# Optimization experiments

Measured on AMD Instinct MI355X. Metric: run time of the kernel, lower is better.

The kernel has to match this reference:

```python
import jax, jax.numpy as jnp
import numpy as np

MARGIN = 0.36
ALPHA_INIT = 0.0
ALPHA_MOMENT = 0.995
LAMBDA_CLEAN = 1.0
LAMBDA_ADV = 1.0
EPS_SIM = 0.01
BIG = 99999.0

CNT = 8192
DIM = 128


def dot_to_dist(dot, alpha, eps=1e-12):
    return alpha * (1.0 - dot) + (1.0 - alpha) * jnp.sqrt(2.0 * (1.0 - dot) + eps)


def find_hard_negatives(dmat):
    # HyNet-style mining: dmat[i, j] = 'distance' between a_i and p_j.
    # Positive pair is the diagonal; hardest negative for triplet i is the min
    # over row i (a_i vs other p) or column i (p_i vs other a), diag excluded.
    cnt = dmat.shape[0]
    dm = dmat + jnp.eye(cnt, dtype=dmat.dtype) * BIG  # mask diagonal
    row_min = dm.min(axis=1)
    row_arg = jnp.argmin(dm, axis=1)
    col_min = dm.min(axis=0)
    col_arg = jnp.argmin(dm, axis=0)
    idx_a = jnp.arange(cnt)
    idx_p = idx_a + cnt
    # indices into cat([a, p]): hardest p lives at j+cnt, hardest a at j
    idx_n = jnp.where(row_min < col_min, row_arg + cnt, col_arg)
    return idx_a, idx_p, idx_n


def estimate_alpha(dots, labels, weights):
    # Vectorized over the 200-point alpha grid (original: Python loop).
    alphas = jnp.arange(-1.0, 1.0, 0.01, dtype=dots.dtype)  # [K=200]
    one_minus = (1.0 - dots)[None, :]                        # [1, N]
    sq = jnp.sqrt(2.0 * (1.0 - dots) + 1e-12)[None, :]       # [1, N]
    dists = alphas[:, None] * one_minus + (1.0 - alphas)[:, None] * sq  # [K, N]
    n = dists.shape[1]
    mean = dists.mean(axis=1, keepdims=True)
    std = jnp.sqrt(((dists - mean) ** 2).sum(axis=1, keepdims=True) / (n - 1))  # unbiased, as torch.std
    probs = jax.nn.sigmoid(-(dists - mean) / std)
    bce = jnp.mean(-labels * jnp.log(probs) * weights
                   - (1.0 - labels) * jnp.log(1.0 - probs) * weights, axis=1)  # [K]
    return alphas[jnp.argmin(bce)]


def _rowdot(x, y):
    return jnp.sum(x * y, axis=1)


def setup_inputs() -> dict:
    key = jax.random.key(0)
    k1, k2, k3 = jax.random.split(key, 3)
    descs = jax.random.normal(k1, (6 * CNT, DIM), dtype=jnp.float32)
    l_a_adv = jax.random.uniform(k2, (CNT,), dtype=jnp.float32)
    l_p_adv = jax.random.uniform(k3, (CNT,), dtype=jnp.float32)
    return {"descs": descs, "l_a_adv": l_a_adv, "l_p_adv": l_p_adv}


def reference(descs, l_a_adv, l_p_adv):
    cnt = descs.shape[0] // 6
    xn = descs / jnp.linalg.norm(descs, axis=1, keepdims=True)
    a     = xn[0 * cnt:1 * cnt]
    p     = xn[1 * cnt:2 * cnt]
    a_rec = xn[2 * cnt:3 * cnt]
    p_rec = xn[3 * cnt:4 * cnt]
    a_adv = xn[4 * cnt:5 * cnt]
    p_adv = xn[5 * cnt:6 * cnt]

    # hard-negative mining (no_grad in original)
    sg = jax.lax.stop_gradient
    smat_ap   = sg(a)     @ sg(p).T       # [cnt, cnt]
    smat_arpa = sg(a_rec) @ sg(p_adv).T
    smat_aapr = sg(a_adv) @ sg(p_rec).T
    idx_a, idx_p, idx_n                = find_hard_negatives(1.0 / smat_ap + EPS_SIM)
    idx_a_arpa, idx_p_arpa, idx_n_arpa = find_hard_negatives(1.0 / smat_arpa + EPS_SIM)
    idx_a_aapr, idx_p_aapr, idx_n_aapr = find_hard_negatives(1.0 / smat_aapr + EPS_SIM)

    xn_ap   = jnp.concatenate([a, p], axis=0)
    xn_arpa = jnp.concatenate([a_rec, p_adv], axis=0)
    xn_aapr = jnp.concatenate([a_adv, p_rec], axis=0)

    pos_ap   = _rowdot(xn_ap[idx_a],        xn_ap[idx_p])
    neg_ap   = _rowdot(xn_ap[idx_a],        xn_ap[idx_n])
    pos_arpa = _rowdot(xn_arpa[idx_a_arpa], xn_arpa[idx_p_arpa])
    neg_arpa = _rowdot(xn_arpa[idx_a_arpa], xn_arpa[idx_n_arpa])
    pos_aapr = _rowdot(xn_aapr[idx_a_aapr], xn_aapr[idx_p_aapr])
    neg_aapr = _rowdot(xn_aapr[idx_a_aapr], xn_aapr[idx_n_aapr])

    acos = lambda d: jnp.arccos(jnp.clip(d, -1.0, 1.0))
    mask = (MARGIN + acos(pos_ap) - acos(neg_ap) > 0).astype(descs.dtype)

    # alpha estimation (no_grad)
    dots = sg(jnp.concatenate([pos_ap, pos_arpa, pos_aapr, neg_ap, neg_arpa, neg_aapr]))
    labels = jnp.concatenate([jnp.ones(cnt * 3, descs.dtype), jnp.zeros(cnt * 3, descs.dtype)])
    weights = jnp.concatenate([
        jnp.full((cnt,), LAMBDA_CLEAN, descs.dtype), jnp.full((2 * cnt,), LAMBDA_ADV, descs.dtype),
        jnp.full((cnt,), LAMBDA_CLEAN, descs.dtype), jnp.full((2 * cnt,), LAMBDA_ADV, descs.dtype)])
    alpha_opt = estimate_alpha(dots, labels, weights)
    alpha = ALPHA_INIT * ALPHA_MOMENT + alpha_opt * (1.0 - ALPHA_MOMENT)

    loss_triplet_clean = jnp.mean((dot_to_dist(pos_ap, alpha) - dot_to_dist(neg_ap, alpha)) * mask) * LAMBDA_CLEAN
    loss_triplet_arpa = jnp.mean((l_p_adv * dot_to_dist(pos_arpa, alpha) - dot_to_dist(neg_arpa, alpha)) * mask) * LAMBDA_ADV
    loss_triplet_aapr = jnp.mean((l_a_adv * dot_to_dist(pos_aapr, alpha) - dot_to_dist(neg_aapr, alpha)) * mask) * LAMBDA_ADV
    loss = jnp.mean(jnp.stack([loss_triplet_clean, loss_triplet_arpa, loss_triplet_aapr]))

    l_mean = (l_a_adv.mean() + l_p_adv.mean()) / 2.0
    mask_ratio = mask.sum() / cnt
    return (loss, loss_triplet_clean, loss_triplet_arpa, loss_triplet_aapr, l_mean, alpha, alpha_opt, mask_ratio)
```

## Files before the change

kernel.cpp:

```cpp
#include <hip/hip_runtime.h>
#include <stdint.h>

#define CNT 8192
#define DIM 128

typedef unsigned long long u64;
typedef unsigned int u32;

#define OFF_POS     ((size_t)0)
#define OFF_NEG     (OFF_POS + (size_t)3*CNT*4)
#define OFF_ROWPART (OFF_NEG + (size_t)3*CNT*4)
#define OFF_COLPART (OFF_ROWPART + (size_t)3*64*CNT*4)
#define OFF_U       (OFF_COLPART + (size_t)3*64*CNT*4)
#define OFF_V       (OFF_U + (size_t)6*CNT*4)
#define OFF_MPART   (OFF_V + (size_t)6*CNT*4)
#define OFF_AMEAN   (OFF_MPART + (size_t)6144*5*4)
#define OFF_AISTD   (OFF_AMEAN + (size_t)1024)
#define OFF_PSUM    (OFF_AISTD + (size_t)1024)
#define OFF_XNB     (OFF_PSUM + (size_t)8192)

typedef __attribute__((ext_vector_type(8))) short short8;
typedef __attribute__((ext_vector_type(4))) float f32x4;

__device__ __forceinline__ float fract1(float x){
#if __has_builtin(__builtin_amdgcn_fractf)
  return __builtin_amdgcn_fractf(x);
#else
  return x - floorf(x);
#endif
}
__device__ __forceinline__ u32 umax2(u32 a, u32 b){ return a > b ? a : b; }
__device__ __forceinline__ u32 umax3(u32 a, u32 b, u32 c){ u32 t = a > b ? a : b; return t > c ? t : c; }

__device__ __forceinline__ float block_sum(float x, float* red, int tid){
  #pragma unroll
  for (int m=1;m<64;m<<=1) x += __shfl_xor(x, m, 64);
  if ((tid & 63) == 0) red[tid>>6] = x;
  __syncthreads();
  const float r = red[0]+red[1]+red[2]+red[3];
  __syncthreads();
  return r;
}

__global__ __launch_bounds__(256) void knorm(const float* __restrict__ in,
                                             unsigned int* __restrict__ xnb32){
  const int row  = blockIdx.x*4 + (threadIdx.x>>6);
  const int lane = threadIdx.x & 63;
  const float2 v = *(const float2*)(in + (size_t)row*DIM + lane*2);
  float ss = v.x*v.x + v.y*v.y;
  #pragma unroll
  for (int m=1;m<64;m<<=1) ss += __shfl_xor(ss, m, 64);
  const float sc = ((row & CNT) ? 1.0f : 0.25f) / sqrtf(ss);
  unsigned int ux = __float_as_uint(v.x*sc), uy = __float_as_uint(v.y*sc);
  ux = (ux + 0x7FFFu + ((ux>>16)&1u)) >> 16;
  uy = (uy + 0x7FFFu + ((uy>>16)&1u)) >> 16;
  xnb32[(size_t)row*64 + lane] = ux | (uy<<16);
}

__global__ __launch_bounds__(256) void kgemm(const unsigned short* __restrict__ xnb,
    u32* __restrict__ rowpart, u32* __restrict__ colpart){
  __shared__ __align__(16) unsigned short S[4][128*32];
  const int pair = blockIdx.z;
  const int xo3[3] = {0, 2*CNT, 4*CNT};
  const int yo3[3] = {CNT, 5*CNT, 3*CNT};
  const unsigned short* __restrict__ X = xnb + (size_t)xo3[pair]*DIM;
  const unsigned short* __restrict__ Y = xnb + (size_t)yo3[pair]*DIM;
  const int brow = blockIdx.y*128, bcol = blockIdx.x*128;
  const int tid = threadIdx.x, lane = tid & 63, wid = tid >> 6;
  const int wr = wid >> 1, wc = wid & 1;
  const int lrow = lane & 15, kgrp = lane >> 4;

  const int j0 = wid*2, j1 = wid*2 + 1;
  const int r0 = j0*16 + (lane>>2), r1 = j1*16 + (lane>>2);
  const int slog = (lane&3) ^ ((lane>>3)&3);
  const unsigned short* gx0 = X + (size_t)(brow + r0)*DIM + slog*8;
  const unsigned short* gx1 = X + (size_t)(brow + r1)*DIM + slog*8;
  const unsigned short* gy0 = Y + (size_t)(bcol + r0)*DIM + slog*8;
  const unsigned short* gy1 = Y + (size_t)(bcol + r1)*DIM + slog*8;

#define STAGEC(c) do{ \
    unsigned short* LX = S[((c)&1)*2]; \
    unsigned short* LY = S[((c)&1)*2 + 1]; \
    __builtin_amdgcn_global_load_lds((const __attribute__((address_space(1))) void*)(gx0 + (c)*32), \
        (__attribute__((address_space(3))) void*)(LX + j0*512), 16, 0, 0); \
    __builtin_amdgcn_global_load_lds((const __attribute__((address_space(1))) void*)(gx1 + (c)*32), \
        (__attribute__((address_space(3))) void*)(LX + j1*512), 16, 0, 0); \
    __builtin_amdgcn_global_load_lds((const __attribute__((address_space(1))) void*)(gy0 + (c)*32), \
        (__attribute__((address_space(3))) void*)(LY + j0*512), 16, 0, 0); \
    __builtin_amdgcn_global_load_lds((const __attribute__((address_space(1))) void*)(gy1 + (c)*32), \
        (__attribute__((address_space(3))) void*)(LY + j1*512), 16, 0, 0); \
  }while(0)

  f32x4 acc[4][4];
  #pragma unroll
  for (int m=0;m<4;m++)
    #pragma unroll
    for (int n=0;n<4;n++)
      acc[m][n] = (f32x4){0.f,0.f,0.f,0.f};

  STAGEC(0);
  __syncthreads();

  const int swzb = ((lrow>>1)&3) << 4;
  #pragma unroll
  for (int c=0;c<4;c++){
    if (c<3) STAGEC(c+1);
    const char* LX = (const char*)S[(c&1)*2];
    const char* LY = (const char*)S[(c&1)*2 + 1];
    const int kb = (kgrp*16) ^ swzb;
    short8 av[4], bv[4];
    #pragma unroll
    for (int m=0;m<4;m++){
      av[m] = *(const short8*)(LX + (wr*64 + m*16 + lrow)*64 + kb);
      bv[m] = *(const short8*)(LY + (wc*64 + m*16 + lrow)*64 + kb);
    }
    #pragma unroll
    for (int m=0;m<4;m++)
      #pragma unroll
      for (int n=0;n<4;n++)
        acc[m][n] = __builtin_amdgcn_mfma_f32_16x16x32_bf16(av[m], bv[n], acc[m][n], 0, 0, 0);
    if (c<3) __syncthreads();
  }

  if (blockIdx.x == blockIdx.y && wr == wc && kgrp == (lrow >> 2)){
    #pragma unroll
    for (int r=0;r<4;r++)
      if ((lrow & 3) == r){
        #pragma unroll
        for (int m=0;m<4;m++) acc[m][m][r] = 0.0f;
      }
  }

  const int colb_loc = wc*64 + lrow;
  u32 orvr[4];
  #pragma unroll
  for (int n=0;n<4;n++) orvr[n] = (u32)(127 - colb_loc - n*16);

  u32 pkc[4] = {0u,0u,0u,0u};
  u32 rpk[16];
  #pragma unroll
  for (int m=0;m<4;m++){
    #pragma unroll
    for (int r=0;r<4;r++){
      const u32 orvc = (u32)(63 - (m*16 + kgrp*4 + r));
      u32 kb2[4];
      #pragma unroll
      for (int n=0;n<4;n++)
        kb2[n] = __float_as_uint(fract1(acc[m][n][r]));
      const u32 b0 = (kb2[0] & 0xFFFFFF80u) | orvr[0];
      const u32 b1 = (kb2[1] & 0xFFFFFF80u) | orvr[1];
      const u32 b2 = (kb2[2] & 0xFFFFFF80u) | orvr[2];
      const u32 b3 = (kb2[3] & 0xFFFFFF80u) | orvr[3];
      rpk[m*4+r] = umax2(umax3(b0, b1, b2), b3);
      const u32 c0 = (kb2[0] & 0xFFFFFFC0u) | orvc;
      const u32 c1 = (kb2[1] & 0xFFFFFFC0u) | orvc;
      const u32 c2 = (kb2[2] & 0xFFFFFFC0u) | orvc;
      const u32 c3 = (kb2[3] & 0xFFFFFFC0u) | orvc;
      pkc[0] = umax2(pkc[0], c0);
      pkc[1] = umax2(pkc[1], c1);
      pkc[2] = umax2(pkc[2], c2);
      pkc[3] = umax2(pkc[3], c3);
    }
  }

  #pragma unroll
  for (int n=0;n<4;n++){
    u32 o = (u32)__shfl_xor((int)pkc[n], 16, 64); pkc[n] = umax2(pkc[n], o);
    o = (u32)__shfl_xor((int)pkc[n], 32, 64);     pkc[n] = umax2(pkc[n], o);
  }

  __syncthreads();
  u32* rowbuf = (u32*)S;
  u32* colred = (u32*)((char*)S + 20480);
  {
    const int slot = wc*16 + lrow;
    #pragma unroll
    for (int m=0;m<4;m++)
      #pragma unroll
      for (int r=0;r<4;r++){
        const int row = wr*64 + m*16 + kgrp*4 + r;
        rowbuf[row*36 + slot] = rpk[m*4+r];
      }
    if (kgrp == 0){
      #pragma unroll
      for (int n=0;n<4;n++)
        colred[wr*128 + wc*64 + n*16 + lrow] = pkc[n];
    }
  }
  __syncthreads();

  if (tid < 128){
    const u32* base = rowbuf + tid*36;
    u32 best = 0u;
    #pragma unroll
    for (int q=0;q<8;q++){
      const uint4 t = *(const uint4*)(base + q*4);
      best = umax2(best, umax2(umax3(t.x, t.y, t.z), t.w));
    }
    const int colg = 127 - (int)(best & 127u);
    rowpart[((size_t)pair*64 + blockIdx.x)*CNT + (brow + tid)] =
        ((~best) & 0xFFFFE000u) | (u32)(bcol + colg);
  } else {
    const int c = tid - 128;
    const u32 a0 = colred[c], a1 = colred[128 + c];
    const u32 w = a1 > a0 ? a1 : a0;
    const int rloc = (a1 > a0 ? 64 : 0) + (63 - (int)(w & 63u));
    colpart[((size_t)pair*64 + blockIdx.y)*CNT + (bcol + c)] =
        ((~w) & 0xFFFFE000u) | (u32)(brow + rloc);
  }
#undef STAGEC
}

__global__ __launch_bounds__(256) void kpick(const float* __restrict__ descs,
    const u32* __restrict__ rowpart, const u32* __restrict__ colpart,
    float* __restrict__ pos, float* __restrict__ neg,
    float* __restrict__ u, float* __restrict__ v, float* __restrict__ mpart){
  __shared__ float sred[4][5];
  const int tid = threadIdx.x;
  const int w4 = tid >> 6, lane = tid & 63;
  const int e = blockIdx.x*4 + w4;
  const int p = e >> 13, i = e & (CNT-1);
  const int xo[3] = {0, 2*CNT, 4*CNT};
  const int yo[3] = {CNT, 5*CNT, 3*CNT};
  u32 rv = rowpart[((size_t)p*64 + lane)*CNT + i];
  u32 cv = colpart[((size_t)p*64 + lane)*CNT + i];
  #pragma unroll
  for (int m=1;m<64;m<<=1){
    u32 o = (u32)__shfl_xor((int)rv, m, 64); rv = o < rv ? o : rv;
    o = (u32)__shfl_xor((int)cv, m, 64);     cv = o < cv ? o : cv;
  }
  int orow;
  if ((rv & 0xFFFFE000u) < (cv & 0xFFFFE000u)) orow = yo[p] + (int)(rv & 0x1FFFu);
  else                                          orow = xo[p] + (int)(cv & 0x1FFFu);
  const float2 va = *(const float2*)(descs + (size_t)(xo[p]+i)*DIM + lane*2);
  const float2 vp = *(const float2*)(descs + (size_t)(yo[p]+i)*DIM + lane*2);
  const float2 vn = *(const float2*)(descs + (size_t)orow*DIM + lane*2);
  float saa = va.x*va.x + va.y*va.y;
  float spp = vp.x*vp.x + vp.y*vp.y;
  float snn = vn.x*vn.x + vn.y*vn.y;
  float sap = va.x*vp.x + va.y*vp.y;
  float san = va.x*vn.x + va.y*vn.y;
  #pragma unroll
  for (int m=1;m<64;m<<=1){
    saa += __shfl_xor(saa, m, 64);
    spp += __shfl_xor(spp, m, 64);
    snn += __shfl_xor(snn, m, 64);
    sap += __shfl_xor(sap, m, 64);
    san += __shfl_xor(san, m, 64);
  }
  if (lane == 0){
    const float dp = sap / (sqrtf(saa)*sqrtf(spp));
    const float dn = san / (sqrtf(saa)*sqrtf(snn));
    pos[p*CNT + i] = dp; neg[p*CNT + i] = dn;
    const float omp_ = 1.f - dp, sqp = sqrtf(2.f*omp_ + 1e-12f), up = omp_ - sqp;
    const float omn_ = 1.f - dn, sqn = sqrtf(2.f*omn_ + 1e-12f), un = omn_ - sqn;
    u[p*CNT + i] = up;           v[p*CNT + i] = sqp;
    u[3*CNT + p*CNT + i] = un;   v[3*CNT + p*CNT + i] = sqn;
    const float cup = up + 0.35f, cvp = sqp - 0.80f;
    const float cun = un + 0.35f, cvn = sqn - 0.80f;
    sred[w4][0] = up + un;
    sred[w4][1] = sqp + sqn;
    sred[w4][2] = cup*cup + cun*cun;
    sred[w4][3] = cup*cvp + cun*cvn;
    sred[w4][4] = cvp*cvp + cvn*cvn;
  }
  __syncthreads();
  if (tid < 5)
    mpart[blockIdx.x*5 + tid] = sred[0][tid] + sred[1][tid] + sred[2][tid] + sred[3][tid];
}

__global__ __launch_bounds__(256) void kmom(const float* __restrict__ mpart,
    float* __restrict__ amean, float* __restrict__ aistd){
  __shared__ float red[4];
  __shared__ float sm[5];
  const int tid = threadIdx.x;
  float a0=0.f,a1=0.f,a2=0.f,a3=0.f,a4=0.f;
  for (int i = tid; i < 6144; i += 256){
    const float* mp = mpart + (size_t)i*5;
    a0+=mp[0]; a1+=mp[1]; a2+=mp[2]; a3+=mp[3]; a4+=mp[4];
  }
  a0 = block_sum(a0, red, tid);
  a1 = block_sum(a1, red, tid);
  a2 = block_sum(a2, red, tid);
  a3 = block_sum(a3, red, tid);
  a4 = block_sum(a4, red, tid);
  if (tid == 0){ sm[0]=a0; sm[1]=a1; sm[2]=a2; sm[3]=a3; sm[4]=a4; }
  __syncthreads();
  const float N = 49152.0f;
  const float mu_u = sm[0]/N, mu_v = sm[1]/N;
  const float du = mu_u + 0.35f, dv = mu_v - 0.80f;
  const float Suu = sm[2] - N*du*du;
  const float Suv = sm[3] - N*du*dv;
  const float Svv = sm[4] - N*dv*dv;
  if (tid < 200){
    const float a = -1.0f + 0.01f*(float)tid;
    amean[tid] = a*mu_u + mu_v;
    const float var = (a*a*Suu + 2.0f*a*Suv + Svv) / 49151.0f;
    aistd[tid] = 1.0f/sqrtf(var);
  }
}

__global__ __launch_bounds__(256) void kbce(const float* __restrict__ u, const float* __restrict__ v,
    const float* __restrict__ amean, const float* __restrict__ aistd, float* __restrict__ psum){
  __shared__ float red[4];
  const int tid = threadIdx.x;
  const int a = blockIdx.x >> 3, c = blockIdx.x & 7;
  const float av = -1.0f + 0.01f*(float)a;
  const float mean = amean[a], istd = aistd[a];
  const int base = c*6144;
  float s = 0.0f;
  #pragma unroll 4
  for (int k = 0; k < 24; ++k){
    const int idx = base + k*256 + tid;
    const float z = (fmaf(av, u[idx], v[idx]) - mean) * istd;
    const float zz = (idx < 3*CNT) ? z : -z;
    s += fmaxf(zz, 0.0f) + __logf(1.0f + __expf(-fabsf(zz)));
  }
  s = block_sum(s, red, tid);
  if (tid == 0) psum[blockIdx.x] = s;
}

__global__ __launch_bounds__(256) void kfinal(const float* __restrict__ pos, const float* __restrict__ neg,
    const float* __restrict__ psum, const float* __restrict__ l_a_adv, const float* __restrict__ l_p_adv,
    float* __restrict__ out){
  __shared__ float sbce[200];
  __shared__ float sal[2];
  __shared__ float red[4];
  const int tid = threadIdx.x;
  if (tid < 200){
    float s = 0.f;
    #pragma unroll
    for (int c=0;c<8;c++) s += psum[tid*8 + c];
    sbce[tid] = s;
  }
  __syncthreads();
  if (tid == 0){
    float best = sbce[0]; int bk = 0;
    for (int k=1;k<200;k++){
      const float vv = sbce[k];
      if (vv < best){ best = vv; bk = k; }
    }
    const float aopt = -1.0f + 0.01f*(float)bk;
    sal[0] = aopt;
    sal[1] = aopt * 0.005f;
  }
  __syncthreads();
  const float alpha = sal[1];

  float sc=0.f, sar=0.f, saa=0.f, sm=0.f, sla=0.f, slp=0.f;
  for (int i = tid; i < CNT; i += 256){
    const float pap = pos[i],        nap = neg[i];
    const float par = pos[CNT+i],    nar = neg[CNT+i];
    const float paa = pos[2*CNT+i],  naa = neg[2*CNT+i];
    const float cp = fminf(fmaxf(pap, -1.0f), 1.0f);
    const float cn = fminf(fmaxf(nap, -1.0f), 1.0f);
    const float m = (0.36f + acosf(cp) - acosf(cn) > 0.0f) ? 1.0f : 0.0f;
    #define DDIST(d) (alpha*(1.0f-(d)) + (1.0f-alpha)*sqrtf(2.0f*(1.0f-(d)) + 1e-12f))
    sc  += (DDIST(pap) - DDIST(nap)) * m;
    sar += (l_p_adv[i]*DDIST(par) - DDIST(nar)) * m;
    saa += (l_a_adv[i]*DDIST(paa) - DDIST(naa)) * m;
    sm  += m;
    sla += l_a_adv[i];
    slp += l_p_adv[i];
  }
  float vals[6] = {sc, sar, saa, sm, sla, slp};
  float tot[6];
  for (int vv=0; vv<6; vv++){
    tot[vv] = block_sum(vals[vv], red, tid);
  }
  if (tid == 0){
    const float lc  = tot[0] / (float)CNT;
    const float lar = tot[1] / (float)CNT;
    const float laa = tot[2] / (float)CNT;
    out[0] = (lc + lar + laa) / 3.0f;
    out[1] = lc;
    out[2] = lar;
    out[3] = laa;
    out[4] = (tot[4]/(float)CNT + tot[5]/(float)CNT) * 0.5f;
    out[5] = sal[1];
    out[6] = sal[0];
    out[7] = tot[3] / (float)CNT;
  }
}

extern "C" void kernel_launch(void* const* d_in, const int* in_sizes, int n_in,
                              void* d_out, int out_size, void* d_ws, size_t ws_size,
                              hipStream_t stream) {
  const float* descs = (const float*)d_in[0];
  const float* l_a   = (const float*)d_in[1];
  const float* l_p   = (const float*)d_in[2];
  float* out = (float*)d_out;
  char* ws = (char*)d_ws;

  float* pos = (float*)(ws + OFF_POS);
  float* neg = (float*)(ws + OFF_NEG);
  u32* rowpart = (u32*)(ws + OFF_ROWPART);
  u32* colpart = (u32*)(ws + OFF_COLPART);
  float* u     = (float*)(ws + OFF_U);
  float* v     = (float*)(ws + OFF_V);
  float* mpart = (float*)(ws + OFF_MPART);
  float* amean = (float*)(ws + OFF_AMEAN);
  float* aistd = (float*)(ws + OFF_AISTD);
  float* psum  = (float*)(ws + OFF_PSUM);
  unsigned int* xnb32 = (unsigned int*)(ws + OFF_XNB);
  const unsigned short* xnb = (const unsigned short*)(ws + OFF_XNB);

  knorm  <<<(6*CNT)/4, 256, 0, stream>>>(descs, xnb32);
  kgemm  <<<dim3(64,64,3), 256, 0, stream>>>(xnb, rowpart, colpart);
  kpick  <<<(3*CNT)/4, 256, 0, stream>>>(descs, rowpart, colpart, pos, neg, u, v, mpart);
  kmom   <<<1, 256, 0, stream>>>(mpart, amean, aistd);
  kbce   <<<1600, 256, 0, stream>>>(u, v, amean, aistd, psum);
  kfinal <<<1, 256, 0, stream>>>(pos, neg, psum, l_a, l_p, out);
}
```

Measured before the change: 156.6 us.

## Enlarge GEMM tile to 256x128 and reuse precomputed inverse norms in pick

The similarity GEMM tile grows from 128x128 to 256x128, so each wave computes 8x4 MFMA tiles. This halves the grid rows and the column-partial buffer, and B fragments are reused across more A rows. Row results are written straight to LDS instead of being held in registers. knorm now stores each row's inverse norm, so kpick computes only two dot products per triplet instead of five reductions. The cost is more accumulator registers and LDS per block, which can lower occupancy.

```diff
diff --git a/kernel.cpp b/kernel.cpp
--- a/kernel.cpp
+++ b/kernel.cpp
@@ -11,7 +11,8 @@
 #define OFF_NEG     (OFF_POS + (size_t)3*CNT*4)
 #define OFF_ROWPART (OFF_NEG + (size_t)3*CNT*4)
 #define OFF_COLPART (OFF_ROWPART + (size_t)3*64*CNT*4)
-#define OFF_U       (OFF_COLPART + (size_t)3*64*CNT*4)
+#define OFF_RNORM   (OFF_COLPART + (size_t)3*32*CNT*4)
+#define OFF_U       (OFF_RNORM + (size_t)6*CNT*4)
 #define OFF_V       (OFF_U + (size_t)6*CNT*4)
 #define OFF_MPART   (OFF_V + (size_t)6*CNT*4)
 #define OFF_AMEAN   (OFF_MPART + (size_t)6144*5*4)
@@ -43,57 +44,65 @@
 }
 
 __global__ __launch_bounds__(256) void knorm(const float* __restrict__ in,
-                                             unsigned int* __restrict__ xnb32){
+                                             unsigned int* __restrict__ xnb32,
+                                             float* __restrict__ rnorm){
   const int row  = blockIdx.x*4 + (threadIdx.x>>6);
   const int lane = threadIdx.x & 63;
   const float2 v = *(const float2*)(in + (size_t)row*DIM + lane*2);
   float ss = v.x*v.x + v.y*v.y;
   #pragma unroll
   for (int m=1;m<64;m<<=1) ss += __shfl_xor(ss, m, 64);
-  const float sc = ((row & CNT) ? 1.0f : 0.25f) / sqrtf(ss);
+  const float rn = 1.0f / sqrtf(ss);
+  const float sc = ((row & CNT) ? 1.0f : 0.25f) * rn;
   unsigned int ux = __float_as_uint(v.x*sc), uy = __float_as_uint(v.y*sc);
   ux = (ux + 0x7FFFu + ((ux>>16)&1u)) >> 16;
   uy = (uy + 0x7FFFu + ((uy>>16)&1u)) >> 16;
   xnb32[(size_t)row*64 + lane] = ux | (uy<<16);
+  if (lane == 0) rnorm[row] = rn;
 }
 
 __global__ __launch_bounds__(256) void kgemm(const unsigned short* __restrict__ xnb,
     u32* __restrict__ rowpart, u32* __restrict__ colpart){
-  __shared__ __align__(16) unsigned short S[4][128*32];
+  __shared__ __align__(16) char LB[49152];
   const int pair = blockIdx.z;
   const int xo3[3] = {0, 2*CNT, 4*CNT};
   const int yo3[3] = {CNT, 5*CNT, 3*CNT};
   const unsigned short* __restrict__ X = xnb + (size_t)xo3[pair]*DIM;
   const unsigned short* __restrict__ Y = xnb + (size_t)yo3[pair]*DIM;
-  const int brow = blockIdx.y*128, bcol = blockIdx.x*128;
+  const int brow = blockIdx.y*256, bcol = blockIdx.x*128;
   const int tid = threadIdx.x, lane = tid & 63, wid = tid >> 6;
   const int wr = wid >> 1, wc = wid & 1;
   const int lrow = lane & 15, kgrp = lane >> 4;
 
-  const int j0 = wid*2, j1 = wid*2 + 1;
-  const int r0 = j0*16 + (lane>>2), r1 = j1*16 + (lane>>2);
+  const int rr16 = lane >> 2;
   const int slog = (lane&3) ^ ((lane>>3)&3);
-  const unsigned short* gx0 = X + (size_t)(brow + r0)*DIM + slog*8;
-  const unsigned short* gx1 = X + (size_t)(brow + r1)*DIM + slog*8;
-  const unsigned short* gy0 = Y + (size_t)(bcol + r0)*DIM + slog*8;
-  const unsigned short* gy1 = Y + (size_t)(bcol + r1)*DIM + slog*8;
+  const unsigned short* gA[4];
+  #pragma unroll
+  for (int t=0;t<4;t++) gA[t] = X + (size_t)(brow + (wid*4+t)*16 + rr16)*DIM + slog*8;
+  const unsigned short* gB[2];
+  #pragma unroll
+  for (int t=0;t<2;t++) gB[t] = Y + (size_t)(bcol + (wid*2+t)*16 + rr16)*DIM + slog*8;
 
 #define STAGEC(c) do{ \
-    unsigned short* LX = S[((c)&1)*2]; \
-    unsigned short* LY = S[((c)&1)*2 + 1]; \
-    __builtin_amdgcn_global_load_lds((const __attribute__((address_space(1))) void*)(gx0 + (c)*32), \
-        (__attribute__((address_space(3))) void*)(LX + j0*512), 16, 0, 0); \
-    __builtin_amdgcn_global_load_lds((const __attribute__((address_space(1))) void*)(gx1 + (c)*32), \
-        (__attribute__((address_space(3))) void*)(LX + j1*512), 16, 0, 0); \
-    __builtin_amdgcn_global_load_lds((const __attribute__((address_space(1))) void*)(gy0 + (c)*32), \
-        (__attribute__((address_space(3))) void*)(LY + j0*512), 16, 0, 0); \
-    __builtin_amdgcn_global_load_lds((const __attribute__((address_space(1))) void*)(gy1 + (c)*32), \
-        (__attribute__((address_space(3))) void*)(LY + j1*512), 16, 0, 0); \
+    char* LA_ = LB + ((c)&1)*16384; \
+    char* LB_ = LB + 32768 + ((c)&1)*8192; \
+    __builtin_amdgcn_global_load_lds((const __attribute__((address_space(1))) void*)(gA[0] + (c)*32), \
+        (__attribute__((address_space(3))) void*)(LA_ + (wid*4+0)*1024), 16, 0, 0); \
+    __builtin_amdgcn_global_load_lds((const __attribute__((address_space(1))) void*)(gA[1] + (c)*32), \
+        (__attribute__((address_space(3))) void*)(LA_ + (wid*4+1)*1024), 16, 0, 0); \
+    __builtin_amdgcn_global_load_lds((const __attribute__((address_space(1))) void*)(gA[2] + (c)*32), \
+        (__attribute__((address_space(3))) void*)(LA_ + (wid*4+2)*1024), 16, 0, 0); \
+    __builtin_amdgcn_global_load_lds((const __attribute__((address_space(1))) void*)(gA[3] + (c)*32), \
+        (__attribute__((address_space(3))) void*)(LA_ + (wid*4+3)*1024), 16, 0, 0); \
+    __builtin_amdgcn_global_load_lds((const __attribute__((address_space(1))) void*)(gB[0] + (c)*32), \
+        (__attribute__((address_space(3))) void*)(LB_ + (wid*2+0)*1024), 16, 0, 0); \
+    __builtin_amdgcn_global_load_lds((const __attribute__((address_space(1))) void*)(gB[1] + (c)*32), \
+        (__attribute__((address_space(3))) void*)(LB_ + (wid*2+1)*1024), 16, 0, 0); \
   }while(0)
 
-  f32x4 acc[4][4];
-  #pragma unroll
-  for (int m=0;m<4;m++)
+  f32x4 acc[8][4];
+  #pragma unroll
+  for (int m=0;m<8;m++)
     #pragma unroll
     for (int n=0;n<4;n++)
       acc[m][n] = (f32x4){0.f,0.f,0.f,0.f};
@@ -101,48 +110,56 @@
   STAGEC(0);
   __syncthreads();
 
-  const int swzb = ((lrow>>1)&3) << 4;
+  const int kb = (kgrp*16) ^ (((lrow>>1)&3) << 4);
   #pragma unroll
   for (int c=0;c<4;c++){
     if (c<3) STAGEC(c+1);
-    const char* LX = (const char*)S[(c&1)*2];
-    const char* LY = (const char*)S[(c&1)*2 + 1];
-    const int kb = (kgrp*16) ^ swzb;
-    short8 av[4], bv[4];
-    #pragma unroll
-    for (int m=0;m<4;m++){
-      av[m] = *(const short8*)(LX + (wr*64 + m*16 + lrow)*64 + kb);
-      bv[m] = *(const short8*)(LY + (wc*64 + m*16 + lrow)*64 + kb);
-    }
-    #pragma unroll
-    for (int m=0;m<4;m++)
+    const char* bA = LB + (c&1)*16384 + (wr*128 + lrow)*64 + kb;
+    const char* bB = LB + 32768 + (c&1)*8192 + (wc*64 + lrow)*64 + kb;
+    short8 bv[4];
+    #pragma unroll
+    for (int n=0;n<4;n++) bv[n] = *(const short8*)(bB + n*1024);
+    #pragma unroll
+    for (int m=0;m<8;m++){
+      const short8 av = *(const short8*)(bA + m*1024);
       #pragma unroll
       for (int n=0;n<4;n++)
-        acc[m][n] = __builtin_amdgcn_mfma_f32_16x16x32_bf16(av[m], bv[n], acc[m][n], 0, 0, 0);
+        acc[m][n] = __builtin_amdgcn_mfma_f32_16x16x32_bf16(av, bv[n], acc[m][n], 0, 0, 0);
+    }
     if (c<3) __syncthreads();
   }
 
-  if (blockIdx.x == blockIdx.y && wr == wc && kgrp == (lrow >> 2)){
+  if ((blockIdx.x >> 1) == blockIdx.y && wr == (int)(blockIdx.x & 1) && kgrp == (lrow >> 2)){
     #pragma unroll
     for (int r=0;r<4;r++)
       if ((lrow & 3) == r){
-        #pragma unroll
-        for (int m=0;m<4;m++) acc[m][m][r] = 0.0f;
+        if (wc == 0){
+          #pragma unroll
+          for (int n=0;n<4;n++) acc[n][n][r] = 0.0f;
+        } else {
+          #pragma unroll
+          for (int n=0;n<4;n++) acc[4+n][n][r] = 0.0f;
+        }
       }
   }
+
+  __syncthreads();
+  u32* rowbuf = (u32*)LB;
+  u32* colred = (u32*)(LB + 40960);
 
   const int colb_loc = wc*64 + lrow;
   u32 orvr[4];
   #pragma unroll
   for (int n=0;n<4;n++) orvr[n] = (u32)(127 - colb_loc - n*16);
-
+  const int rowbase = wr*128 + kgrp*4;
+  const int slot = wc*16 + lrow;
   u32 pkc[4] = {0u,0u,0u,0u};
-  u32 rpk[16];
-  #pragma unroll
-  for (int m=0;m<4;m++){
+  #pragma unroll
+  for (int m=0;m<8;m++){
     #pragma unroll
     for (int r=0;r<4;r++){
-      const u32 orvc = (u32)(63 - (m*16 + kgrp*4 + r));
+      const int rowloc = rowbase + m*16 + r;
+      const u32 orvc = (u32)(255 - rowloc);
       u32 kb2[4];
       #pragma unroll
       for (int n=0;n<4;n++)
@@ -151,15 +168,11 @@
       const u32 b1 = (kb2[1] & 0xFFFFFF80u) | orvr[1];
       const u32 b2 = (kb2[2] & 0xFFFFFF80u) | orvr[2];
       const u32 b3 = (kb2[3] & 0xFFFFFF80u) | orvr[3];
-      rpk[m*4+r] = umax2(umax3(b0, b1, b2), b3);
-      const u32 c0 = (kb2[0] & 0xFFFFFFC0u) | orvc;
-      const u32 c1 = (kb2[1] & 0xFFFFFFC0u) | orvc;
-      const u32 c2 = (kb2[2] & 0xFFFFFFC0u) | orvc;
-      const u32 c3 = (kb2[3] & 0xFFFFFFC0u) | orvc;
-      pkc[0] = umax2(pkc[0], c0);
-      pkc[1] = umax2(pkc[1], c1);
-      pkc[2] = umax2(pkc[2], c2);
-      pkc[3] = umax2(pkc[3], c3);
+      rowbuf[rowloc*36 + slot] = umax2(umax3(b0, b1, b2), b3);
+      pkc[0] = umax2(pkc[0], (kb2[0] & 0xFFFFFF00u) | orvc);
+      pkc[1] = umax2(pkc[1], (kb2[1] & 0xFFFFFF00u) | orvc);
+      pkc[2] = umax2(pkc[2], (kb2[2] & 0xFFFFFF00u) | orvc);
+      pkc[3] = umax2(pkc[3], (kb2[3] & 0xFFFFFF00u) | orvc);
     }
   }
 
@@ -168,28 +181,14 @@
     u32 o = (u32)__shfl_xor((int)pkc[n], 16, 64); pkc[n] = umax2(pkc[n], o);
     o = (u32)__shfl_xor((int)pkc[n], 32, 64);     pkc[n] = umax2(pkc[n], o);
   }
-
-  __syncthreads();
-  u32* rowbuf = (u32*)S;
-  u32* colred = (u32*)((char*)S + 20480);
+  if (kgrp == 0){
+    #pragma unroll
+    for (int n=0;n<4;n++)
+      colred[wr*128 + wc*64 + n*16 + lrow] = pkc[n];
+  }
+  __syncthreads();
+
   {
-    const int slot = wc*16 + lrow;
-    #pragma unroll
-    for (int m=0;m<4;m++)
-      #pragma unroll
-      for (int r=0;r<4;r++){
-        const int row = wr*64 + m*16 + kgrp*4 + r;
-        rowbuf[row*36 + slot] = rpk[m*4+r];
-      }
-    if (kgrp == 0){
-      #pragma unroll
-      for (int n=0;n<4;n++)
-        colred[wr*128 + wc*64 + n*16 + lrow] = pkc[n];
-    }
-  }
-  __syncthreads();
-
-  if (tid < 128){
     const u32* base = rowbuf + tid*36;
     u32 best = 0u;
     #pragma unroll
@@ -200,18 +199,19 @@
     const int colg = 127 - (int)(best & 127u);
     rowpart[((size_t)pair*64 + blockIdx.x)*CNT + (brow + tid)] =
         ((~best) & 0xFFFFE000u) | (u32)(bcol + colg);
-  } else {
-    const int c = tid - 128;
-    const u32 a0 = colred[c], a1 = colred[128 + c];
-    const u32 w = a1 > a0 ? a1 : a0;
-    const int rloc = (a1 > a0 ? 64 : 0) + (63 - (int)(w & 63u));
-    colpart[((size_t)pair*64 + blockIdx.y)*CNT + (bcol + c)] =
+  }
+  if (tid < 128){
+    const u32 a0 = colred[tid], a1 = colred[128 + tid];
+    const u32 w = umax2(a0, a1);
+    const int rloc = 255 - (int)(w & 255u);
+    colpart[((size_t)pair*32 + blockIdx.y)*CNT + (bcol + tid)] =
         ((~w) & 0xFFFFE000u) | (u32)(brow + rloc);
   }
 #undef STAGEC
 }
 
 __global__ __launch_bounds__(256) void kpick(const float* __restrict__ descs,
+    const float* __restrict__ rnorm,
     const u32* __restrict__ rowpart, const u32* __restrict__ colpart,
     float* __restrict__ pos, float* __restrict__ neg,
     float* __restrict__ u, float* __restrict__ v, float* __restrict__ mpart){
@@ -223,7 +223,7 @@
   const int xo[3] = {0, 2*CNT, 4*CNT};
   const int yo[3] = {CNT, 5*CNT, 3*CNT};
   u32 rv = rowpart[((size_t)p*64 + lane)*CNT + i];
-  u32 cv = colpart[((size_t)p*64 + lane)*CNT + i];
+  u32 cv = (lane < 32) ? colpart[((size_t)p*32 + lane)*CNT + i] : 0xFFFFFFFFu;
   #pragma unroll
   for (int m=1;m<64;m<<=1){
     u32 o = (u32)__shfl_xor((int)rv, m, 64); rv = o < rv ? o : rv;
@@ -235,22 +235,17 @@
   const float2 va = *(const float2*)(descs + (size_t)(xo[p]+i)*DIM + lane*2);
   const float2 vp = *(const float2*)(descs + (size_t)(yo[p]+i)*DIM + lane*2);
   const float2 vn = *(const float2*)(descs + (size_t)orow*DIM + lane*2);
-  float saa = va.x*va.x + va.y*va.y;
-  float spp = vp.x*vp.x + vp.y*vp.y;
-  float snn = vn.x*vn.x + vn.y*vn.y;
   float sap = va.x*vp.x + va.y*vp.y;
   float san = va.x*vn.x + va.y*vn.y;
   #pragma unroll
   for (int m=1;m<64;m<<=1){
-    saa += __shfl_xor(saa, m, 64);
-    spp += __shfl_xor(spp, m, 64);
-    snn += __shfl_xor(snn, m, 64);
     sap += __shfl_xor(sap, m, 64);
     san += __shfl_xor(san, m, 64);
   }
   if (lane == 0){
-    const float dp = sap / (sqrtf(saa)*sqrtf(spp));
-    const float dn = san / (sqrtf(saa)*sqrtf(snn));
+    const float rna = rnorm[xo[p]+i];
+    const float dp = sap * rna * rnorm[yo[p]+i];
+    const float dn = san * rna * rnorm[orow];
     pos[p*CNT + i] = dp; neg[p*CNT + i] = dn;
     const float omp_ = 1.f - dp, sqp = sqrtf(2.f*omp_ + 1e-12f), up = omp_ - sqp;
     const float omn_ = 1.f - dn, sqn = sqrtf(2.f*omn_ + 1e-12f), un = omn_ - sqn;
@@ -396,6 +391,7 @@
   float* neg = (float*)(ws + OFF_NEG);
   u32* rowpart = (u32*)(ws + OFF_ROWPART);
   u32* colpart = (u32*)(ws + OFF_COLPART);
+  float* rnorm = (float*)(ws + OFF_RNORM);
   float* u     = (float*)(ws + OFF_U);
   float* v     = (float*)(ws + OFF_V);
   float* mpart = (float*)(ws + OFF_MPART);
@@ -405,9 +401,9 @@
   unsigned int* xnb32 = (unsigned int*)(ws + OFF_XNB);
   const unsigned short* xnb = (const unsigned short*)(ws + OFF_XNB);
 
-  knorm  <<<(6*CNT)/4, 256, 0, stream>>>(descs, xnb32);
-  kgemm  <<<dim3(64,64,3), 256, 0, stream>>>(xnb, rowpart, colpart);
-  kpick  <<<(3*CNT)/4, 256, 0, stream>>>(descs, rowpart, colpart, pos, neg, u, v, mpart);
+  knorm  <<<(6*CNT)/4, 256, 0, stream>>>(descs, xnb32, rnorm);
+  kgemm  <<<dim3(64,32,3), 256, 0, stream>>>(xnb, rowpart, colpart);
+  kpick  <<<(3*CNT)/4, 256, 0, stream>>>(descs, rnorm, rowpart, colpart, pos, neg, u, v, mpart);
   kmom   <<<1, 256, 0, stream>>>(mpart, amean, aistd);
   kbce   <<<1600, 256, 0, stream>>>(u, v, amean, aistd, psum);
   kfinal <<<1, 256, 0, stream>>>(pos, neg, psum, l_a, l_p, out);
```

Result: slower. 197.8 us (+26.3%).
